# Performance work log

Hardware: AMD Instinct MI355X
Metric: run time of the kernel (lower is better)

## Reference

```python
import jax, jax.numpy as jnp
import numpy as np

EPS = 1e-5      # BatchNorm eps
QLEV = 255.0    # 8-bit PACT activation levels (unsigned)
WMAX = 127.0    # int8 symmetric weight range


def _ste(x, q):
    # straight-through estimator: forward value q, gradient of x
    return x + jax.lax.stop_gradient(q - x)


def _wquant(w):
    # channel-wise symmetric int8 fake-quant of conv weights (per out-channel)
    s = jnp.maximum(jnp.max(jnp.abs(w), axis=(1, 2, 3), keepdims=True) / WMAX, 1e-8)
    q = jnp.clip(jnp.round(w / s), -WMAX, WMAX) * s
    return _ste(w, q)


def _conv3x3(x, w, stride=1):
    return jax.lax.conv_general_dilated(
        x, w, window_strides=(stride, stride), padding=((1, 1), (1, 1)),
        dimension_numbers=("NCHW", "OIHW", "NCHW"))


def _bn(x, g, b, m, v):
    # folded BatchNorm: per-channel affine with running stats
    return (x - m) * (g * jax.lax.rsqrt(v + EPS)) + b


def _pact(x, alpha):
    # PACT: clip to [0, alpha] then 8-bit per-channel fake-quant
    c = jnp.clip(x, 0.0, alpha)
    s = alpha / QLEV
    q = jnp.round(c / s) * s
    return _ste(c, q)


def _requant(x, s):
    # requantize onto common grid s (shift-based align in the int model)
    return _ste(x, jnp.round(x / s) * s)


def setup_inputs() -> dict:
    key = jax.random.key(0)
    ks = jax.random.split(key, 10)
    N, C, H, W = 32, 128, 56, 56
    x = jax.random.normal(ks[0], (N, C, H, W), jnp.float32)
    w1 = jax.random.normal(ks[1], (C, C, 3, 3), jnp.float32) * 0.05
    w2 = jax.random.normal(ks[2], (C, C, 3, 3), jnp.float32) * 0.05
    pc = (1, C, 1, 1)
    g1 = jnp.ones(pc, jnp.float32); b1 = jnp.zeros(pc, jnp.float32)
    m1 = jax.random.normal(ks[3], pc, jnp.float32) * 0.1
    v1 = jax.random.uniform(ks[4], pc, jnp.float32) + 0.5
    g2 = jnp.ones(pc, jnp.float32); b2 = jnp.zeros(pc, jnp.float32)
    m2 = jax.random.normal(ks[5], pc, jnp.float32) * 0.1
    v2 = jax.random.uniform(ks[6], pc, jnp.float32) + 0.5
    a1 = jax.random.uniform(ks[7], pc, jnp.float32) * 2.0 + 2.0
    a2 = jax.random.uniform(ks[8], pc, jnp.float32) * 2.0 + 2.0
    a3 = jax.random.uniform(ks[9], pc, jnp.float32) * 2.0 + 2.0
    return {"x": x, "w1": w1, "g1": g1, "b1": b1, "m1": m1, "v1": v1, "a1": a1,
            "w2": w2, "g2": g2, "b2": b2, "m2": m2, "v2": v2, "a2": a2, "a3": a3}


def reference(x, w1, g1, b1, m1, v1, a1, w2, g2, b2, m2, v2, a2, a3):
    # branch: quant-conv -> BN -> PACT-quant, twice
    out = _pact(_bn(_conv3x3(x, _wquant(w1)), g1, b1, m1, v1), a1)
    out = _pact(_bn(_conv3x3(out, _wquant(w2)), g2, b2, m2, v2), a2)
    # shift-based residual add: align both operands to act3's quant grid, add, clip+quant
    s3 = a3 / QLEV
    y = _requant(out, s3) + _requant(x, s3)
    return _pact(y, a3)
```

## Files before the change

kernel.cpp:

```cpp
#include <hip/hip_runtime.h>
#include <cstdint>

typedef __attribute__((ext_vector_type(4))) float f32x4;
typedef __attribute__((ext_vector_type(2))) float f32x2;
typedef __attribute__((ext_vector_type(4))) int int4v;
typedef __attribute__((ext_vector_type(4))) uint32_t uint4v;

#define EPSV 1e-5f

#define IMG   3136
#define NPIX  100352
#define PADTOT 13778944
#define S1Q (8.0f/127.0f)
#define S2Q (8.0f/(127.0f*254.0f))
#define S1A (4.0f/127.0f)
#define S2A (4.0f/(127.0f*254.0f))

__global__ __launch_bounds__(256) void k_prep(
    const float* __restrict__ x, const float* __restrict__ w1, const float* __restrict__ w2,
    const float* __restrict__ g1, const float* __restrict__ b1, const float* __restrict__ m1,
    const float* __restrict__ v1, const float* __restrict__ a1,
    const float* __restrict__ g2, const float* __restrict__ b2, const float* __restrict__ m2,
    const float* __restrict__ v2, const float* __restrict__ a2, const float* __restrict__ a3,
    int8_t* __restrict__ xq1, int8_t* __restrict__ xq2,
    int8_t* __restrict__ wj1, int8_t* __restrict__ wj2,
    char* __restrict__ o1k1, char* __restrict__ o1k2,
    f32x4* __restrict__ pp1, f32x4* __restrict__ pp2, f32x4* __restrict__ pp3,
    short* __restrict__ j3, int use_j3) {
  __shared__ float shf[7296];
  const int bid = blockIdx.x;
  const int t = threadIdx.x;

  if (bid < 1792) {
    int n = bid / 56, h = bid - (bid / 56) * 56;
    const float* base = x + (size_t)n * 401408 + h * 56;
    for (int idx = t; idx < 7168; idx += 256) {
      int ci = idx / 56, w = idx - (idx / 56) * 56;
      shf[ci * 57 + w] = base[ci * 3136 + w];
    }
    __syncthreads();
    const int ob = ((n * 58 + h + 1) * 58 + 1) * 128;
    for (int idx = t; idx < 1792; idx += 256) {
      int w = idx >> 5, c4 = (idx & 31) * 4;
      uint32_t p1 = 0, p2 = 0;
#pragma unroll
      for (int j = 0; j < 4; ++j) {
        float v = shf[(c4 + j) * 57 + w];
        float j1 = rintf(v * (127.0f / 8.0f));
        j1 = fminf(fmaxf(j1, -127.f), 127.f);
        float rr = v - j1 * S1Q;
        float j2 = rintf(rr * ((127.0f * 254.0f) / 8.0f));
        j2 = fminf(fmaxf(j2, -127.f), 127.f);
        p1 |= ((uint32_t)((int)j1 & 0xff)) << (8 * j);
        p2 |= ((uint32_t)((int)j2 & 0xff)) << (8 * j);
      }
      *(uint32_t*)(xq1 + ob + w * 128 + c4) = p1;
      *(uint32_t*)(xq2 + ob + w * 128 + c4) = p2;
    }
    if (use_j3) {
      const size_t jb = (size_t)n * 401408 + h * 56;
      for (int idx = t; idx < 7168; idx += 256) {
        int ci = idx / 56, w = idx - (idx / 56) * 56;
        float inv3 = 255.0f / a3[ci];
        j3[jb + ci * 3136 + w] = (short)(int)rintf(shf[ci * 57 + w] * inv3);
      }
    }
  } else if (bid < 1792 + 912) {
    int i = (bid - 1792) * 256 + t;
    int bi = i / 58368;
    int j = i - bi * 58368;
    char* buf = (bi == 0) ? (char*)xq1 : (bi == 1) ? (char*)xq2 : (bi == 2) ? o1k1 : o1k2;
    int n = j / 1824, cid = j - n * 1824;
    const int rowc = 58 * 8;
    int chunk;
    if (cid < rowc) chunk = cid;
    else if (cid < 2 * rowc) chunk = 57 * rowc + (cid - rowc);
    else {
      int e = cid - 2 * rowc;
      int h = 1 + (e >> 4);
      int r = e & 15;
      int w = (r < 8) ? 0 : 57;
      chunk = h * rowc + w * 8 + (r & 7);
    }
    long addr = ((long)n * 26912 + chunk) * 16;
    *(uint4v*)(buf + addr) = (uint4v){0u, 0u, 0u, 0u};
  } else if (bid < 1792 + 912 + 256) {
    int sub = bid - 2704;
    int o = sub & 127;
    bool second = sub >= 128;
    const float* src = (second ? w2 : w1) + o * 1152;
    int8_t* wj = second ? wj2 : wj1;
    float* red = shf;
    float m = 0.f;
    for (int i = t; i < 1152; i += 256) m = fmaxf(m, fabsf(src[i]));
    red[t] = m;
    __syncthreads();
    for (int s = 128; s > 0; s >>= 1) {
      if (t < s) red[t] = fmaxf(red[t], red[t + s]);
      __syncthreads();
    }
    float s = fmaxf(red[0] / 127.0f, 1e-8f);
    for (int i = t; i < 1152; i += 256) {
      float q = rintf(src[i] / s);
      q = fminf(fmaxf(q, -127.f), 127.f);
      int ci = i / 9, tap = i - ci * 9;
      wj[(tap * 128 + o) * 128 + ci] = (int8_t)(int)q;
    }
  } else {
    if (t < 128) {
      float mx1 = 0.f, mx2 = 0.f;
      const float* p1w = w1 + t * 1152;
      const float* p2w = w2 + t * 1152;
      for (int i = 0; i < 1152; ++i) {
        mx1 = fmaxf(mx1, fabsf(p1w[i]));
        mx2 = fmaxf(mx2, fabsf(p2w[i]));
      }
      float s1w = fmaxf(mx1 / 127.0f, 1e-8f);
      float s2w = fmaxf(mx2 / 127.0f, 1e-8f);
      float r1 = 1.0f / sqrtf(v1[t] + EPSV);
      float sc1 = g1[t] * r1;
      pp1[t] = (f32x4){s1w * sc1, b1[t] - m1[t] * sc1, 255.0f / a1[t], a1[t] / 255.0f};
      float r2 = 1.0f / sqrtf(v2[t] + EPSV);
      float sc2 = g2[t] * r2;
      pp2[t] = (f32x4){s2w * sc2, b2[t] - m2[t] * sc2, 255.0f / a2[t], a2[t] / 255.0f};
      pp3[t] = (f32x4){a3[t] / 255.0f, 255.0f / a3[t], a3[t], 0.0f};
    }
  }
}

__global__ __launch_bounds__(256, 2) void k_conv1(
    const int8_t* __restrict__ xq1, const int8_t* __restrict__ xq2,
    const int8_t* __restrict__ wj1, const f32x4* __restrict__ pp1,
    int8_t* __restrict__ o1k1, int8_t* __restrict__ o1k2) {
  __shared__ char smem[49152];
  char* Al = smem;
  char* Bh = smem + 16384;
  char* Bl = smem + 32768;
  const int t = threadIdx.x;
  const int l = t & 63;
  const int wv = t >> 6;
  const int wr = wv >> 1, wc = wv & 1;
  const int lane15 = l & 15, hi4 = l >> 4;
  const int px0 = blockIdx.x * 128;
  const int srow = t >> 3, sl = t & 7;

  int pixbase[4];
#pragma unroll
  for (int r = 0; r < 4; ++r) {
    unsigned gpx = px0 + srow + 32 * r;
    unsigned n = gpx / IMG;
    unsigned rem = gpx - n * IMG;
    unsigned h = rem / 56;
    unsigned w = rem - h * 56;
    pixbase[r] = (int)(((n * 58u + h) * 58u + w) * 128u) + sl * 16;
  }

  int4v acc1[4][4], acc2[4][4];
#pragma unroll
  for (int i = 0; i < 4; ++i)
#pragma unroll
    for (int j = 0; j < 4; ++j) { acc1[i][j] = (int4v){0,0,0,0}; acc2[i][j] = (int4v){0,0,0,0}; }

  int4v av[4], bhv[4], blv[4];
#pragma unroll
  for (int r = 0; r < 4; ++r) {
    const int row = srow + 32 * r;
    av[r]  = *(const int4v*)(wj1 + row * 128 + sl * 16);
    bhv[r] = *(const int4v*)(xq1 + pixbase[r]);
    blv[r] = *(const int4v*)(xq2 + pixbase[r]);
  }

#pragma unroll 1
  for (int tap = 0; tap < 9; ++tap) {
    __syncthreads();
#pragma unroll
    for (int r = 0; r < 4; ++r) {
      const int row = srow + 32 * r;
      const int ss = row * 128 + ((sl ^ (row & 7)) * 16);
      *(int4v*)&Al[ss] = av[r];
      *(int4v*)&Bh[ss] = bhv[r];
      *(int4v*)&Bl[ss] = blv[r];
    }
    __syncthreads();
    if (tap < 8) {
      const int nt = tap + 1;
      const int kh = nt / 3, kw = nt - kh * 3;
      const int tapoff = (kh * 58 + kw) * 128;
#pragma unroll
      for (int r = 0; r < 4; ++r) {
        const int row = srow + 32 * r;
        av[r]  = *(const int4v*)(wj1 + (nt * 128 + row) * 128 + sl * 16);
        bhv[r] = *(const int4v*)(xq1 + pixbase[r] + tapoff);
        blv[r] = *(const int4v*)(xq2 + pixbase[r] + tapoff);
      }
    }
#pragma unroll
    for (int kk = 0; kk < 2; ++kk) {
      int4v a[4];
#pragma unroll
      for (int m = 0; m < 4; ++m) {
        const int row = wr * 64 + m * 16 + lane15;
        a[m] = *(const int4v*)&Al[row * 128 + (((kk * 4 + hi4) ^ (row & 7)) * 16)];
      }
      int4v bv[4];
#pragma unroll
      for (int n2 = 0; n2 < 4; ++n2) {
        const int row = wc * 64 + n2 * 16 + lane15;
        bv[n2] = *(const int4v*)&Bh[row * 128 + (((kk * 4 + hi4) ^ (row & 7)) * 16)];
      }
#pragma unroll
      for (int m = 0; m < 4; ++m)
#pragma unroll
        for (int n2 = 0; n2 < 4; ++n2)
          acc1[m][n2] = __builtin_amdgcn_mfma_i32_16x16x64_i8(a[m], bv[n2], acc1[m][n2], 0, 0, 0);
#pragma unroll
      for (int n2 = 0; n2 < 4; ++n2) {
        const int row = wc * 64 + n2 * 16 + lane15;
        bv[n2] = *(const int4v*)&Bl[row * 128 + (((kk * 4 + hi4) ^ (row & 7)) * 16)];
      }
#pragma unroll
      for (int m = 0; m < 4; ++m)
#pragma unroll
        for (int n2 = 0; n2 < 4; ++n2)
          acc2[m][n2] = __builtin_amdgcn_mfma_i32_16x16x64_i8(a[m], bv[n2], acc2[m][n2], 0, 0, 0);
    }
  }

  __syncthreads();
  char* sT1 = smem;
  char* sT2 = smem + 16384;
#pragma unroll
  for (int m = 0; m < 4; ++m) {
    const int cobase = wr * 64 + m * 16 + 4 * hi4;
    const int slot = cobase >> 4, off = cobase & 15;
#pragma unroll
    for (int n2 = 0; n2 < 4; ++n2) {
      const int pxl = wc * 64 + n2 * 16 + lane15;
      uint32_t pk1 = 0, pk2 = 0;
#pragma unroll
      for (int r = 0; r < 4; ++r) {
        f32x4 p = pp1[cobase + r];
        float accf = (float)acc1[m][n2][r] * S1Q + (float)acc2[m][n2][r] * S2Q;
        float y = accf * p[0] + p[1];
        float cv = fminf(fmaxf(y, 0.f), p[3] * 255.0f);
        float act = rintf(cv * p[2]) * p[3];
        float k1 = fminf(rintf(act * (127.0f / 4.0f)), 127.f);
        float rr = act - k1 * S1A;
        float k2 = fminf(fmaxf(rintf(rr * ((127.0f * 254.0f) / 4.0f)), -127.f), 127.f);
        pk1 |= ((uint32_t)((int)k1 & 0xff)) << (8 * r);
        pk2 |= ((uint32_t)((int)k2 & 0xff)) << (8 * r);
      }
      const int ad = pxl * 128 + ((slot ^ (pxl & 7)) * 16) + off;
      *(uint32_t*)&sT1[ad] = pk1;
      *(uint32_t*)&sT2[ad] = pk2;
    }
  }
  __syncthreads();
  {
    const int pxl = t >> 1, half = t & 1;
    unsigned gpx = px0 + pxl;
    unsigned n = gpx / IMG;
    unsigned rem = gpx - n * IMG;
    unsigned h = rem / 56;
    unsigned w = rem - h * 56;
    int ob = (int)(((n * 58u + h + 1u) * 58u + (w + 1u)) * 128u) + half * 64;
#pragma unroll
    for (int i = 0; i < 4; ++i) {
      const int slot = half * 4 + i;
      const int ad = pxl * 128 + ((slot ^ (pxl & 7)) * 16);
      uint4v v1 = *(uint4v*)&sT1[ad];
      uint4v v2 = *(uint4v*)&sT2[ad];
      *(uint4v*)(o1k1 + ob + i * 16) = v1;
      *(uint4v*)(o1k2 + ob + i * 16) = v2;
    }
  }
}

__global__ __launch_bounds__(256, 2) void k_conv2(
    const int8_t* __restrict__ o1k1, const int8_t* __restrict__ o1k2,
    const int8_t* __restrict__ wj2, const f32x4* __restrict__ pp2,
    const f32x4* __restrict__ pp3, const float* __restrict__ x,
    const short* __restrict__ j3, int use_j3,
    float* __restrict__ out) {
  __shared__ char smem[49152];
  char* Al = smem;
  char* Bh = smem + 16384;
  char* Bl = smem + 32768;
  const int t = threadIdx.x;
  const int l = t & 63;
  const int wv = t >> 6;
  const int wr = wv >> 1, wc = wv & 1;
  const int lane15 = l & 15, hi4 = l >> 4;
  const int px0 = blockIdx.x * 128;
  const int srow = t >> 3, sl = t & 7;

  int pixbase[4];
#pragma unroll
  for (int r = 0; r < 4; ++r) {
    unsigned gpx = px0 + srow + 32 * r;
    unsigned n = gpx / IMG;
    unsigned rem = gpx - n * IMG;
    unsigned h = rem / 56;
    unsigned w = rem - h * 56;
    pixbase[r] = (int)(((n * 58u + h) * 58u + w) * 128u) + sl * 16;
  }

  int4v acc1[4][4], acc2[4][4];
#pragma unroll
  for (int i = 0; i < 4; ++i)
#pragma unroll
    for (int j = 0; j < 4; ++j) { acc1[i][j] = (int4v){0,0,0,0}; acc2[i][j] = (int4v){0,0,0,0}; }

  int4v av[4], bhv[4], blv[4];
#pragma unroll
  for (int r = 0; r < 4; ++r) {
    const int row = srow + 32 * r;
    av[r]  = *(const int4v*)(wj2 + row * 128 + sl * 16);
    bhv[r] = *(const int4v*)(o1k1 + pixbase[r]);
    blv[r] = *(const int4v*)(o1k2 + pixbase[r]);
  }

#pragma unroll 1
  for (int tap = 0; tap < 9; ++tap) {
    __syncthreads();
#pragma unroll
    for (int r = 0; r < 4; ++r) {
      const int row = srow + 32 * r;
      const int ss = row * 128 + ((sl ^ (row & 7)) * 16);
      *(int4v*)&Al[ss] = av[r];
      *(int4v*)&Bh[ss] = bhv[r];
      *(int4v*)&Bl[ss] = blv[r];
    }
    __syncthreads();
    if (tap < 8) {
      const int nt = tap + 1;
      const int kh = nt / 3, kw = nt - kh * 3;
      const int tapoff = (kh * 58 + kw) * 128;
#pragma unroll
      for (int r = 0; r < 4; ++r) {
        const int row = srow + 32 * r;
        av[r]  = *(const int4v*)(wj2 + (nt * 128 + row) * 128 + sl * 16);
        bhv[r] = *(const int4v*)(o1k1 + pixbase[r] + tapoff);
        blv[r] = *(const int4v*)(o1k2 + pixbase[r] + tapoff);
      }
    }
#pragma unroll
    for (int kk = 0; kk < 2; ++kk) {
      int4v a[4];
#pragma unroll
      for (int m = 0; m < 4; ++m) {
        const int row = wr * 64 + m * 16 + lane15;
        a[m] = *(const int4v*)&Al[row * 128 + (((kk * 4 + hi4) ^ (row & 7)) * 16)];
      }
      int4v bv[4];
#pragma unroll
      for (int n2 = 0; n2 < 4; ++n2) {
        const int row = wc * 64 + n2 * 16 + lane15;
        bv[n2] = *(const int4v*)&Bh[row * 128 + (((kk * 4 + hi4) ^ (row & 7)) * 16)];
      }
#pragma unroll
      for (int m = 0; m < 4; ++m)
#pragma unroll
        for (int n2 = 0; n2 < 4; ++n2)
          acc1[m][n2] = __builtin_amdgcn_mfma_i32_16x16x64_i8(a[m], bv[n2], acc1[m][n2], 0, 0, 0);
#pragma unroll
      for (int n2 = 0; n2 < 4; ++n2) {
        const int row = wc * 64 + n2 * 16 + lane15;
        bv[n2] = *(const int4v*)&Bl[row * 128 + (((kk * 4 + hi4) ^ (row & 7)) * 16)];
      }
#pragma unroll
      for (int m = 0; m < 4; ++m)
#pragma unroll
        for (int n2 = 0; n2 < 4; ++n2)
          acc2[m][n2] = __builtin_amdgcn_mfma_i32_16x16x64_i8(a[m], bv[n2], acc2[m][n2], 0, 0, 0);
    }
  }

  __syncthreads();
  float* E = (float*)smem;
  const int pxl2 = l * 2;
  unsigned gpx0 = px0 + pxl2;
  unsigned nn = gpx0 / IMG;
  unsigned rrem = gpx0 - nn * IMG;
  const size_t obase = (size_t)nn * 401408 + rrem;

#pragma unroll
  for (int m = 0; m < 4; ++m) {
#pragma unroll
    for (int n2 = 0; n2 < 4; ++n2) {
      const int pxl = wc * 64 + n2 * 16 + lane15;
#pragma unroll
      for (int r = 0; r < 4; ++r) {
        const int co_l = wr * 16 + 4 * hi4 + r;
        E[co_l * 132 + pxl] = (float)acc1[m][n2][r] * S1A + (float)acc2[m][n2][r] * S2A;
      }
    }
    __syncthreads();
#pragma unroll
    for (int cid = 0; cid < 8; ++cid) {
      const int co_l = wv * 8 + cid;
      const int co = m * 16 + (co_l < 16 ? co_l : co_l + 48);
      const f32x4 p2 = pp2[co];
      const f32x4 p3 = pp3[co];
      const size_t off = obase + (size_t)co * 3136;
      float v0 = E[co_l * 132 + pxl2];
      float v1 = E[co_l * 132 + pxl2 + 1];
      float rx0, rx1;
      if (use_j3) {
        const short* jp = j3 + off;
        rx0 = (float)jp[0] * p3[0];
        rx1 = (float)jp[1] * p3[0];
      } else {
        const float* xp = x + off;
        rx0 = rintf(xp[0] * p3[1]) * p3[0];
        rx1 = rintf(xp[1] * p3[1]) * p3[0];
      }
      float o0, o1;
      {
        float y = v0 * p2[0] + p2[1];
        float cv = fminf(fmaxf(y, 0.f), p2[3] * 255.0f);
        float act = rintf(cv * p2[2]) * p2[3];
        float ro = rintf(act * p3[1]) * p3[0];
        float y3 = ro + rx0;
        float c3 = fminf(fmaxf(y3, 0.f), p3[2]);
        o0 = rintf(c3 * p3[1]) * p3[0];
      }
      {
        float y = v1 * p2[0] + p2[1];
        float cv = fminf(fmaxf(y, 0.f), p2[3] * 255.0f);
        float act = rintf(cv * p2[2]) * p2[3];
        float ro = rintf(act * p3[1]) * p3[0];
        float y3 = ro + rx1;
        float c3 = fminf(fmaxf(y3, 0.f), p3[2]);
        o1 = rintf(c3 * p3[1]) * p3[0];
      }
      *(f32x2*)(out + off) = (f32x2){o0, o1};
    }
    __syncthreads();
  }
}

extern "C" void kernel_launch(void* const* d_in, const int* in_sizes, int n_in,
                              void* d_out, int out_size, void* d_ws, size_t ws_size,
                              hipStream_t stream) {
  (void)in_sizes; (void)n_in; (void)out_size;
  const float* x  = (const float*)d_in[0];
  const float* w1 = (const float*)d_in[1];
  const float* g1 = (const float*)d_in[2];
  const float* b1 = (const float*)d_in[3];
  const float* m1 = (const float*)d_in[4];
  const float* v1 = (const float*)d_in[5];
  const float* a1 = (const float*)d_in[6];
  const float* w2 = (const float*)d_in[7];
  const float* g2 = (const float*)d_in[8];
  const float* b2 = (const float*)d_in[9];
  const float* m2 = (const float*)d_in[10];
  const float* v2 = (const float*)d_in[11];
  const float* a2 = (const float*)d_in[12];
  const float* a3 = (const float*)d_in[13];

  char* ws = (char*)d_ws;
  int8_t* xq1  = (int8_t*)ws;
  int8_t* xq2  = (int8_t*)(ws + (size_t)PADTOT);
  int8_t* o1k1 = (int8_t*)(ws + 2 * (size_t)PADTOT);
  int8_t* o1k2 = (int8_t*)(ws + 3 * (size_t)PADTOT);
  int8_t* wj1  = (int8_t*)(ws + 4 * (size_t)PADTOT);
  int8_t* wj2  = (int8_t*)(ws + 4 * (size_t)PADTOT + 147456);
  f32x4*  pp1  = (f32x4*)(ws + 4 * (size_t)PADTOT + 2 * 147456);
  f32x4*  pp2  = pp1 + 128;
  f32x4*  pp3  = pp2 + 128;
  size_t j3off = 4 * (size_t)PADTOT + 2 * 147456 + 16384;
  short*  j3   = (short*)(ws + j3off);
  size_t need  = j3off + (size_t)NPIX * 128 * 2;
  int use_j3 = (ws_size >= need) ? 1 : 0;

  k_prep<<<2961, 256, 0, stream>>>(x, w1, w2, g1, b1, m1, v1, a1, g2, b2, m2, v2, a2, a3,
                                   xq1, xq2, wj1, wj2, (char*)o1k1, (char*)o1k2,
                                   pp1, pp2, pp3, j3, use_j3);
  k_conv1<<<784, 256, 0, stream>>>(xq1, xq2, wj1, pp1, o1k1, o1k2);
  k_conv2<<<784, 256, 0, stream>>>(o1k1, o1k2, wj2, pp2, pp3, x, j3, use_j3, (float*)d_out);
}
```

Measured before the change: 184.8 us.

## Load MFMA operands directly from global memory, drop LDS staging in convs

Both conv kernels now load A (weights) and B (activation) fragments straight from global memory into registers in MFMA layout, double-buffered per half-K. This removes LDS staging and the two barriers per tap. Blocks are also remapped so consecutive block IDs cover spread-out pixel tiles. The serial per-channel parameter block in the prep kernel is folded into the weight-quant blocks, which removes one straggler block. The cost is redundant global and L2 reads, since each wave fetches its own fragments instead of sharing them through LDS, plus higher register pressure.

Measured after the change: 274.3 us. +48.4%, slower.

```diff
diff --git a/kernel.cpp b/kernel.cpp
--- a/kernel.cpp
+++ b/kernel.cpp
@@ -15,6 +15,11 @@
 #define S2Q (8.0f/(127.0f*254.0f))
 #define S1A (4.0f/127.0f)
 #define S2A (4.0f/(127.0f*254.0f))
+
+#define MFMA_TILE(aarr, barr, accarr)                                            \
+  _Pragma("unroll") for (int m_ = 0; m_ < 4; ++m_)                               \
+  _Pragma("unroll") for (int n_ = 0; n_ < 4; ++n_)                               \
+    accarr[m_][n_] = __builtin_amdgcn_mfma_i32_16x16x64_i8(aarr[m_], barr[n_], accarr[m_][n_], 0, 0, 0);
 
 __global__ __launch_bounds__(256) void k_prep(
     const float* __restrict__ x, const float* __restrict__ w1, const float* __restrict__ w2,
@@ -84,7 +89,7 @@
     }
     long addr = ((long)n * 26912 + chunk) * 16;
     *(uint4v*)(buf + addr) = (uint4v){0u, 0u, 0u, 0u};
-  } else if (bid < 1792 + 912 + 256) {
+  } else {
     int sub = bid - 2704;
     int o = sub & 127;
     bool second = sub >= 128;
@@ -106,24 +111,17 @@
       int ci = i / 9, tap = i - ci * 9;
       wj[(tap * 128 + o) * 128 + ci] = (int8_t)(int)q;
     }
-  } else {
-    if (t < 128) {
-      float mx1 = 0.f, mx2 = 0.f;
-      const float* p1w = w1 + t * 1152;
-      const float* p2w = w2 + t * 1152;
-      for (int i = 0; i < 1152; ++i) {
-        mx1 = fmaxf(mx1, fabsf(p1w[i]));
-        mx2 = fmaxf(mx2, fabsf(p2w[i]));
-      }
-      float s1w = fmaxf(mx1 / 127.0f, 1e-8f);
-      float s2w = fmaxf(mx2 / 127.0f, 1e-8f);
-      float r1 = 1.0f / sqrtf(v1[t] + EPSV);
-      float sc1 = g1[t] * r1;
-      pp1[t] = (f32x4){s1w * sc1, b1[t] - m1[t] * sc1, 255.0f / a1[t], a1[t] / 255.0f};
-      float r2 = 1.0f / sqrtf(v2[t] + EPSV);
-      float sc2 = g2[t] * r2;
-      pp2[t] = (f32x4){s2w * sc2, b2[t] - m2[t] * sc2, 255.0f / a2[t], a2[t] / 255.0f};
-      pp3[t] = (f32x4){a3[t] / 255.0f, 255.0f / a3[t], a3[t], 0.0f};
+    if (t == 0) {
+      if (!second) {
+        float r1 = 1.0f / sqrtf(v1[o] + EPSV);
+        float sc1 = g1[o] * r1;
+        pp1[o] = (f32x4){s * sc1, b1[o] - m1[o] * sc1, 255.0f / a1[o], a1[o] / 255.0f};
+        pp3[o] = (f32x4){a3[o] / 255.0f, 255.0f / a3[o], a3[o], 0.0f};
+      } else {
+        float r2 = 1.0f / sqrtf(v2[o] + EPSV);
+        float sc2 = g2[o] * r2;
+        pp2[o] = (f32x4){s * sc2, b2[o] - m2[o] * sc2, 255.0f / a2[o], a2[o] / 255.0f};
+      }
     }
   }
 }
@@ -132,28 +130,26 @@
     const int8_t* __restrict__ xq1, const int8_t* __restrict__ xq2,
     const int8_t* __restrict__ wj1, const f32x4* __restrict__ pp1,
     int8_t* __restrict__ o1k1, int8_t* __restrict__ o1k2) {
-  __shared__ char smem[49152];
-  char* Al = smem;
-  char* Bh = smem + 16384;
-  char* Bl = smem + 32768;
+  __shared__ char smem[32768];
   const int t = threadIdx.x;
   const int l = t & 63;
   const int wv = t >> 6;
   const int wr = wv >> 1, wc = wv & 1;
   const int lane15 = l & 15, hi4 = l >> 4;
-  const int px0 = blockIdx.x * 128;
-  const int srow = t >> 3, sl = t & 7;
-
-  int pixbase[4];
-#pragma unroll
-  for (int r = 0; r < 4; ++r) {
-    unsigned gpx = px0 + srow + 32 * r;
+  const int bid = blockIdx.x;
+  const int px0 = ((bid & 7) * 98 + (bid >> 3)) * 128;
+
+  int pb[4];
+#pragma unroll
+  for (int n2 = 0; n2 < 4; ++n2) {
+    unsigned gpx = px0 + wc * 64 + n2 * 16 + lane15;
     unsigned n = gpx / IMG;
     unsigned rem = gpx - n * IMG;
     unsigned h = rem / 56;
     unsigned w = rem - h * 56;
-    pixbase[r] = (int)(((n * 58u + h) * 58u + w) * 128u) + sl * 16;
-  }
+    pb[n2] = (int)(((n * 58u + h) * 58u + w) * 128u) + hi4 * 16;
+  }
+  const int aoff0 = (wr * 64 + lane15) * 128 + hi4 * 16;
 
   int4v acc1[4][4], acc2[4][4];
 #pragma unroll
@@ -161,72 +157,44 @@
 #pragma unroll
     for (int j = 0; j < 4; ++j) { acc1[i][j] = (int4v){0,0,0,0}; acc2[i][j] = (int4v){0,0,0,0}; }
 
-  int4v av[4], bhv[4], blv[4];
+  int4v a[4], bh0[4], bl0[4], bh1[4], bl1[4];
 #pragma unroll
   for (int r = 0; r < 4; ++r) {
-    const int row = srow + 32 * r;
-    av[r]  = *(const int4v*)(wj1 + row * 128 + sl * 16);
-    bhv[r] = *(const int4v*)(xq1 + pixbase[r]);
-    blv[r] = *(const int4v*)(xq2 + pixbase[r]);
+    bh0[r] = *(const int4v*)(xq1 + pb[r]);
+    bl0[r] = *(const int4v*)(xq2 + pb[r]);
   }
 
 #pragma unroll 1
   for (int tap = 0; tap < 9; ++tap) {
-    __syncthreads();
+    const int kh = tap / 3, kw = tap - kh * 3;
+    const int toff = (kh * 58 + kw) * 128;
+#pragma unroll
+    for (int m = 0; m < 4; ++m)
+      a[m] = *(const int4v*)(wj1 + tap * 16384 + aoff0 + m * 2048);
 #pragma unroll
     for (int r = 0; r < 4; ++r) {
-      const int row = srow + 32 * r;
-      const int ss = row * 128 + ((sl ^ (row & 7)) * 16);
-      *(int4v*)&Al[ss] = av[r];
-      *(int4v*)&Bh[ss] = bhv[r];
-      *(int4v*)&Bl[ss] = blv[r];
-    }
-    __syncthreads();
+      bh1[r] = *(const int4v*)(xq1 + pb[r] + toff + 64);
+      bl1[r] = *(const int4v*)(xq2 + pb[r] + toff + 64);
+    }
+    MFMA_TILE(a, bh0, acc1)
+    MFMA_TILE(a, bl0, acc2)
+#pragma unroll
+    for (int m = 0; m < 4; ++m)
+      a[m] = *(const int4v*)(wj1 + tap * 16384 + 64 + aoff0 + m * 2048);
     if (tap < 8) {
       const int nt = tap + 1;
-      const int kh = nt / 3, kw = nt - kh * 3;
-      const int tapoff = (kh * 58 + kw) * 128;
+      const int nkh = nt / 3, nkw = nt - nkh * 3;
+      const int ntoff = (nkh * 58 + nkw) * 128;
 #pragma unroll
       for (int r = 0; r < 4; ++r) {
-        const int row = srow + 32 * r;
-        av[r]  = *(const int4v*)(wj1 + (nt * 128 + row) * 128 + sl * 16);
-        bhv[r] = *(const int4v*)(xq1 + pixbase[r] + tapoff);
-        blv[r] = *(const int4v*)(xq2 + pixbase[r] + tapoff);
-      }
-    }
-#pragma unroll
-    for (int kk = 0; kk < 2; ++kk) {
-      int4v a[4];
-#pragma unroll
-      for (int m = 0; m < 4; ++m) {
-        const int row = wr * 64 + m * 16 + lane15;
-        a[m] = *(const int4v*)&Al[row * 128 + (((kk * 4 + hi4) ^ (row & 7)) * 16)];
-      }
-      int4v bv[4];
-#pragma unroll
-      for (int n2 = 0; n2 < 4; ++n2) {
-        const int row = wc * 64 + n2 * 16 + lane15;
-        bv[n2] = *(const int4v*)&Bh[row * 128 + (((kk * 4 + hi4) ^ (row & 7)) * 16)];
-      }
-#pragma unroll
-      for (int m = 0; m < 4; ++m)
-#pragma unroll
-        for (int n2 = 0; n2 < 4; ++n2)
-          acc1[m][n2] = __builtin_amdgcn_mfma_i32_16x16x64_i8(a[m], bv[n2], acc1[m][n2], 0, 0, 0);
-#pragma unroll
-      for (int n2 = 0; n2 < 4; ++n2) {
-        const int row = wc * 64 + n2 * 16 + lane15;
-        bv[n2] = *(const int4v*)&Bl[row * 128 + (((kk * 4 + hi4) ^ (row & 7)) * 16)];
-      }
-#pragma unroll
-      for (int m = 0; m < 4; ++m)
-#pragma unroll
-        for (int n2 = 0; n2 < 4; ++n2)
-          acc2[m][n2] = __builtin_amdgcn_mfma_i32_16x16x64_i8(a[m], bv[n2], acc2[m][n2], 0, 0, 0);
-    }
-  }
-
-  __syncthreads();
+        bh0[r] = *(const int4v*)(xq1 + pb[r] + ntoff);
+        bl0[r] = *(const int4v*)(xq2 + pb[r] + ntoff);
+      }
+    }
+    MFMA_TILE(a, bh1, acc1)
+    MFMA_TILE(a, bl1, acc2)
+  }
+
   char* sT1 = smem;
   char* sT2 = smem + 16384;
 #pragma unroll
@@ -282,28 +250,26 @@
     const f32x4* __restrict__ pp3, const float* __restrict__ x,
     const short* __restrict__ j3, int use_j3,
     float* __restrict__ out) {
-  __shared__ char smem[49152];
-  char* Al = smem;
-  char* Bh = smem + 16384;
-  char* Bl = smem + 32768;
+  __shared__ float E[4224];
   const int t = threadIdx.x;
   const int l = t & 63;
   const int wv = t >> 6;
   const int wr = wv >> 1, wc = wv & 1;
   const int lane15 = l & 15, hi4 = l >> 4;
-  const int px0 = blockIdx.x * 128;
-  const int srow = t >> 3, sl = t & 7;
-
-  int pixbase[4];
-#pragma unroll
-  for (int r = 0; r < 4; ++r) {
-    unsigned gpx = px0 + srow + 32 * r;
+  const int bid = blockIdx.x;
+  const int px0 = ((bid & 7) * 98 + (bid >> 3)) * 128;
+
+  int pb[4];
+#pragma unroll
+  for (int n2 = 0; n2 < 4; ++n2) {
+    unsigned gpx = px0 + wc * 64 + n2 * 16 + lane15;
     unsigned n = gpx / IMG;
     unsigned rem = gpx - n * IMG;
     unsigned h = rem / 56;
     unsigned w = rem - h * 56;
-    pixbase[r] = (int)(((n * 58u + h) * 58u + w) * 128u) + sl * 16;
-  }
+    pb[n2] = (int)(((n * 58u + h) * 58u + w) * 128u) + hi4 * 16;
+  }
+  const int aoff0 = (wr * 64 + lane15) * 128 + hi4 * 16;
 
   int4v acc1[4][4], acc2[4][4];
 #pragma unroll
@@ -311,73 +277,44 @@
 #pragma unroll
     for (int j = 0; j < 4; ++j) { acc1[i][j] = (int4v){0,0,0,0}; acc2[i][j] = (int4v){0,0,0,0}; }
 
-  int4v av[4], bhv[4], blv[4];
+  int4v a[4], bh0[4], bl0[4], bh1[4], bl1[4];
 #pragma unroll
   for (int r = 0; r < 4; ++r) {
-    const int row = srow + 32 * r;
-    av[r]  = *(const int4v*)(wj2 + row * 128 + sl * 16);
-    bhv[r] = *(const int4v*)(o1k1 + pixbase[r]);
-    blv[r] = *(const int4v*)(o1k2 + pixbase[r]);
+    bh0[r] = *(const int4v*)(o1k1 + pb[r]);
+    bl0[r] = *(const int4v*)(o1k2 + pb[r]);
   }
 
 #pragma unroll 1
   for (int tap = 0; tap < 9; ++tap) {
-    __syncthreads();
+    const int kh = tap / 3, kw = tap - kh * 3;
+    const int toff = (kh * 58 + kw) * 128;
+#pragma unroll
+    for (int m = 0; m < 4; ++m)
+      a[m] = *(const int4v*)(wj2 + tap * 16384 + aoff0 + m * 2048);
 #pragma unroll
     for (int r = 0; r < 4; ++r) {
-      const int row = srow + 32 * r;
-      const int ss = row * 128 + ((sl ^ (row & 7)) * 16);
-      *(int4v*)&Al[ss] = av[r];
-      *(int4v*)&Bh[ss] = bhv[r];
-      *(int4v*)&Bl[ss] = blv[r];
-    }
-    __syncthreads();
+      bh1[r] = *(const int4v*)(o1k1 + pb[r] + toff + 64);
+      bl1[r] = *(const int4v*)(o1k2 + pb[r] + toff + 64);
+    }
+    MFMA_TILE(a, bh0, acc1)
+    MFMA_TILE(a, bl0, acc2)
+#pragma unroll
+    for (int m = 0; m < 4; ++m)
+      a[m] = *(const int4v*)(wj2 + tap * 16384 + 64 + aoff0 + m * 2048);
     if (tap < 8) {
       const int nt = tap + 1;
-      const int kh = nt / 3, kw = nt - kh * 3;
-      const int tapoff = (kh * 58 + kw) * 128;
+      const int nkh = nt / 3, nkw = nt - nkh * 3;
+      const int ntoff = (nkh * 58 + nkw) * 128;
 #pragma unroll
       for (int r = 0; r < 4; ++r) {
-        const int row = srow + 32 * r;
-        av[r]  = *(const int4v*)(wj2 + (nt * 128 + row) * 128 + sl * 16);
-        bhv[r] = *(const int4v*)(o1k1 + pixbase[r] + tapoff);
-        blv[r] = *(const int4v*)(o1k2 + pixbase[r] + tapoff);
-      }
-    }
-#pragma unroll
-    for (int kk = 0; kk < 2; ++kk) {
-      int4v a[4];
-#pragma unroll
-      for (int m = 0; m < 4; ++m) {
-        const int row = wr * 64 + m * 16 + lane15;
-        a[m] = *(const int4v*)&Al[row * 128 + (((kk * 4 + hi4) ^ (row & 7)) * 16)];
-      }
-      int4v bv[4];
-#pragma unroll
-      for (int n2 = 0; n2 < 4; ++n2) {
-        const int row = wc * 64 + n2 * 16 + lane15;
-        bv[n2] = *(const int4v*)&Bh[row * 128 + (((kk * 4 + hi4) ^ (row & 7)) * 16)];
-      }
-#pragma unroll
-      for (int m = 0; m < 4; ++m)
-#pragma unroll
-        for (int n2 = 0; n2 < 4; ++n2)
-          acc1[m][n2] = __builtin_amdgcn_mfma_i32_16x16x64_i8(a[m], bv[n2], acc1[m][n2], 0, 0, 0);
-#pragma unroll
-      for (int n2 = 0; n2 < 4; ++n2) {
-        const int row = wc * 64 + n2 * 16 + lane15;
-        bv[n2] = *(const int4v*)&Bl[row * 128 + (((kk * 4 + hi4) ^ (row & 7)) * 16)];
-      }
-#pragma unroll
-      for (int m = 0; m < 4; ++m)
-#pragma unroll
-        for (int n2 = 0; n2 < 4; ++n2)
-          acc2[m][n2] = __builtin_amdgcn_mfma_i32_16x16x64_i8(a[m], bv[n2], acc2[m][n2], 0, 0, 0);
-    }
-  }
-
-  __syncthreads();
-  float* E = (float*)smem;
+        bh0[r] = *(const int4v*)(o1k1 + pb[r] + ntoff);
+        bl0[r] = *(const int4v*)(o1k2 + pb[r] + ntoff);
+      }
+    }
+    MFMA_TILE(a, bh1, acc1)
+    MFMA_TILE(a, bl1, acc2)
+  }
+
   const int pxl2 = l * 2;
   unsigned gpx0 = px0 + pxl2;
   unsigned nn = gpx0 / IMG;
@@ -474,7 +411,7 @@
   size_t need  = j3off + (size_t)NPIX * 128 * 2;
   int use_j3 = (ws_size >= need) ? 1 : 0;
 
-  k_prep<<<2961, 256, 0, stream>>>(x, w1, w2, g1, b1, m1, v1, a1, g2, b2, m2, v2, a2, a3,
+  k_prep<<<2960, 256, 0, stream>>>(x, w1, w2, g1, b1, m1, v1, a1, g2, b2, m2, v2, a2, a3,
                                    xq1, xq2, wj1, wj2, (char*)o1k1, (char*)o1k2,
                                    pp1, pp2, pp3, j3, use_j3);
   k_conv1<<<784, 256, 0, stream>>>(xq1, xq2, wj1, pp1, o1k1, o1k2);
```
